# Performance work log

Hardware: AMD Instinct MI355X
Metric: run time of the kernel (lower is better)

The kernel has to match this reference:

```python
import jax, jax.numpy as jnp
import numpy as np

BS, S, D, H, KVH, HD = 2, 2048, 2048, 32, 8, 64
N_REP = H // KVH
N_DOCS = 4


def setup_inputs() -> dict:
    key = jax.random.key(0)
    ks = jax.random.split(key, 7)
    x = jax.random.normal(ks[0], (BS, S, D), dtype=jnp.float32)
    # RoPE table (llama theta=10000), stored as real (cos, sin) pairs: [S, HD//2, 2]
    inv_freq = 1.0 / (10000.0 ** (jnp.arange(0, HD, 2, dtype=jnp.float32) / HD))
    ang = jnp.arange(S, dtype=jnp.float32)[:, None] * inv_freq[None, :]  # [S, HD//2]
    freqs_cis = jnp.stack([jnp.cos(ang), jnp.sin(ang)], axis=-1)
    # packed-document ids, non-decreasing along sequence: [BS, S]
    sequence_id = jnp.sort(
        jax.random.randint(ks[1], (BS, S), 0, N_DOCS, dtype=jnp.int32), axis=-1
    )
    std = 0.02
    wq = jax.random.normal(ks[2], (H * HD, D), dtype=jnp.float32) * std
    wk = jax.random.normal(ks[3], (KVH * HD, D), dtype=jnp.float32) * std
    wv = jax.random.normal(ks[4], (KVH * HD, D), dtype=jnp.float32) * std
    wo = jax.random.normal(ks[5], (D, H * HD), dtype=jnp.float32) * std
    return {"x": x, "freqs_cis": freqs_cis, "sequence_id": sequence_id,
            "wq": wq, "wk": wk, "wv": wv, "wo": wo}


def _apply_rope(t, freqs_cis):
    # t: [b, s, h, hd]; freqs_cis: [s, hd//2, 2] (cos, sin)
    b, s, h, hd = t.shape
    tp = t.reshape(b, s, h, hd // 2, 2)
    t0, t1 = tp[..., 0], tp[..., 1]
    cos = freqs_cis[None, :, None, :, 0]
    sin = freqs_cis[None, :, None, :, 1]
    o0 = t0 * cos - t1 * sin
    o1 = t0 * sin + t1 * cos
    return jnp.stack([o0, o1], axis=-1).reshape(b, s, h, hd)


def reference(x, freqs_cis, sequence_id, wq, wk, wv, wo):
    bs, s, _ = x.shape
    xq = (x @ wq.T).reshape(bs, s, H, HD)
    xk = (x @ wk.T).reshape(bs, s, KVH, HD)
    xv = (x @ wv.T).reshape(bs, s, KVH, HD)
    xq = _apply_rope(xq, freqs_cis)
    xk = _apply_rope(xk, freqs_cis)
    # GQA without materializing repeated KV: group queries by kv head
    q = xq.reshape(bs, s, KVH, N_REP, HD).transpose(0, 2, 3, 1, 4)  # [b,g,r,s,d]
    k = xk.transpose(0, 2, 1, 3)  # [b,g,s,d]
    v = xv.transpose(0, 2, 1, 3)  # [b,g,s,d]
    scale = 1.0 / jnp.sqrt(jnp.float32(HD))
    scores = jnp.einsum("bgrqd,bgkd->bgrqk", q, k) * scale
    # document-causal mask: same sequence_id AND causal
    causal = jnp.tril(jnp.ones((s, s), dtype=bool))
    same_doc = sequence_id[:, :, None] == sequence_id[:, None, :]  # [b,s,s]
    mask = (causal[None] & same_doc)[:, None, None, :, :]  # [b,1,1,s,s]
    scores = jnp.where(mask, scores, jnp.float32(-1e30))
    probs = jax.nn.softmax(scores, axis=-1)
    out = jnp.einsum("bgrqk,bgkd->bgrqd", probs, v)  # [b,g,r,s,d]
    out = out.transpose(0, 3, 1, 2, 4).reshape(bs, s, H * HD)
    return out @ wo.T
```

## Files before the change

### kernel.cpp

```cpp
#include <hip/hip_runtime.h>
#include <hip/hip_bf16.h>

typedef __attribute__((ext_vector_type(8))) short bf16x8;
typedef __attribute__((ext_vector_type(4))) float f32x4;

#define MFMA16(A, B, C) __builtin_amdgcn_mfma_f32_16x16x32_bf16(A, B, C, 0, 0, 0)

__device__ __forceinline__ unsigned short f2bf(float f) {
    unsigned int u = __float_as_uint(f);
    u += 0x7fffu + ((u >> 16) & 1u);
    return (unsigned short)(u >> 16);
}
__device__ __forceinline__ float bf2f(unsigned short h) {
    return __uint_as_float(((unsigned int)h) << 16);
}
__device__ __forceinline__ unsigned int pack_bf2(float lo, float hi) {
    __hip_bfloat162 h = __float22bfloat162_rn(make_float2(lo, hi));
    return *reinterpret_cast<unsigned int*>(&h);
}

__device__ __forceinline__ void gload_lds16(const void* g, void* l) {
    __builtin_amdgcn_global_load_lds(
        (__attribute__((address_space(1))) unsigned int*)g,
        (__attribute__((address_space(3))) unsigned int*)l, 16, 0, 0);
}

__global__ void cvt_kernel(const float* __restrict__ in, unsigned short* __restrict__ out, int n4) {
    const int i = blockIdx.x * 256 + threadIdx.x;
    if (i >= n4) return;
    const float4 v = ((const float4*)in)[i];
    uint2 o;
    o.x = pack_bf2(v.x, v.y);
    o.y = pack_bf2(v.z, v.w);
    ((uint2*)out)[i] = o;
}

__global__ void docstart_kernel(const int* __restrict__ sid, int* __restrict__ ds) {
    const int i = blockIdx.x * 256 + threadIdx.x;
    const int b = i >> 11, s = i & 2047;
    const int* row = sid + b * 2048;
    const int v = row[s];
    int lo = 0, hi = s;
    while (lo < hi) { const int mid = (lo + hi) >> 1; if (row[mid] < v) lo = mid + 1; else hi = mid; }
    ds[i] = lo;
}

template <int EPI>
__global__ __launch_bounds__(256) void gemm_bt(
    const unsigned short* __restrict__ A,
    const unsigned short* __restrict__ B,
    int K, int N,
    unsigned short* __restrict__ oq,
    unsigned short* __restrict__ ok,
    unsigned short* __restrict__ ov,
    float* __restrict__ of)
{
    __shared__ __align__(16) unsigned short sA[128 * 32];
    __shared__ __align__(16) unsigned short sB[128 * 32];
    const int tid = threadIdx.x;
    const int lane = tid & 63, wave = tid >> 6;
    const int wr = wave >> 1, wc = wave & 1;
    const int lr = lane & 15, lc = lane >> 4;

    int bid = blockIdx.y * gridDim.x + blockIdx.x;
    const int cpx = (gridDim.x * gridDim.y) >> 3;
    bid = (bid & 7) * cpx + (bid >> 3);
    const int m0 = (bid / gridDim.x) * 128, n0 = (bid % gridDim.x) * 128;

    f32x4 acc[4][4];
#pragma unroll
    for (int i = 0; i < 4; i++)
#pragma unroll
        for (int j = 0; j < 4; j++) acc[i][j] = (f32x4){0.f, 0.f, 0.f, 0.f};

    const int u0 = tid, u1 = tid + 256;
    for (int k0 = 0; k0 < K; k0 += 32) {
        __syncthreads();
        gload_lds16(A + (size_t)(m0 + (u0 >> 2)) * K + k0 + (u0 & 3) * 8, &sA[u0 * 8]);
        gload_lds16(A + (size_t)(m0 + (u1 >> 2)) * K + k0 + (u1 & 3) * 8, &sA[u1 * 8]);
        gload_lds16(B + (size_t)(n0 + (u0 >> 2)) * K + k0 + (u0 & 3) * 8, &sB[u0 * 8]);
        gload_lds16(B + (size_t)(n0 + (u1 >> 2)) * K + k0 + (u1 & 3) * 8, &sB[u1 * 8]);
        __syncthreads();
        bf16x8 af[4], bfv[4];
#pragma unroll
        for (int i = 0; i < 4; i++) {
            af[i]  = *(const bf16x8*)&sA[(wr * 64 + i * 16 + lr) * 32 + lc * 8];
            bfv[i] = *(const bf16x8*)&sB[(wc * 64 + i * 16 + lr) * 32 + lc * 8];
        }
#pragma unroll
        for (int i = 0; i < 4; i++)
#pragma unroll
            for (int j = 0; j < 4; j++) acc[i][j] = MFMA16(af[i], bfv[j], acc[i][j]);
    }

    if (EPI == 0) {
#pragma unroll
        for (int i = 0; i < 4; i++) {
#pragma unroll
            for (int j = 0; j < 4; j++) {
                const int n = n0 + wc * 64 + j * 16 + lr;
                const int d = n & 63;
#pragma unroll
                for (int r = 0; r < 4; r++) {
                    const int m = m0 + wr * 64 + i * 16 + lc * 4 + r;
                    const int bb = m >> 11, s = m & 2047;
                    const unsigned short val = f2bf(acc[i][j][r]);
                    if (n < 2048) {
                        const int hh = n >> 6;
                        oq[((((size_t)bb * 32 + hh) * 2048 + s) << 6) + d] = val;
                    } else if (n < 2560) {
                        const int hh = (n >> 6) - 32;
                        ok[((((size_t)bb * 8 + hh) * 2048 + s) << 6) + d] = val;
                    } else {
                        const int hh = (n >> 6) - 40;
                        ov[((((size_t)bb * 8 + hh) * 2048 + s) << 6) + d] = val;
                    }
                }
            }
        }
    } else {
#pragma unroll
        for (int i = 0; i < 4; i++)
#pragma unroll
            for (int j = 0; j < 4; j++)
#pragma unroll
                for (int r = 0; r < 4; r++) {
                    const int m = m0 + wr * 64 + i * 16 + lc * 4 + r;
                    const int n = n0 + wc * 64 + j * 16 + lr;
                    of[(size_t)m * N + n] = acc[i][j][r];
                }
    }
}

__global__ void rope_kernel(unsigned short* __restrict__ Qb,
                            unsigned short* __restrict__ Kb,
                            const float* __restrict__ fc)
{
    const int NQ = 2 * 32 * 2048 * 32;
    int i = blockIdx.x * 256 + threadIdx.x;
    unsigned short* base;
    if (i < NQ) base = Qb;
    else { base = Kb; i -= NQ; }
    const int p = i & 31, s = (i >> 5) & 2047, bh = i >> 16;
    const size_t off = (((size_t)bh * 2048 + s) << 6) + p * 2;
    const unsigned int w = *(const unsigned int*)&base[off];
    const float t0 = bf2f((unsigned short)(w & 0xffffu));
    const float t1 = bf2f((unsigned short)(w >> 16));
    const float c = fc[(s * 32 + p) * 2], sn = fc[(s * 32 + p) * 2 + 1];
    *(unsigned int*)&base[off] = pack_bf2(t0 * c - t1 * sn, t0 * sn + t1 * c);
}

__global__ __launch_bounds__(256) void attn_kernel(
    const unsigned short* __restrict__ Q,
    const unsigned short* __restrict__ K,
    const unsigned short* __restrict__ V,
    const int* __restrict__ dstart,
    unsigned short* __restrict__ AO)
{
    const int qt = 31 - blockIdx.x;
    const int h = blockIdx.y, b = blockIdx.z;
    const int kvh = h >> 2;
    const int tid = threadIdx.x, lane = tid & 63, wave = tid >> 6;
    const int lr = lane & 15, lc = lane >> 4;
    const int q0 = qt * 64;
    const int qw = q0 + wave * 16;

    __shared__ __align__(16) unsigned short sK[64 * 64];
    __shared__ __align__(16) unsigned short sVt[64][72];

    const unsigned short* Qh = Q + (((size_t)b * 32 + h) * 2048) * 64;
    const unsigned short* Kh = K + (((size_t)b * 8 + kvh) * 2048) * 64;
    const unsigned short* Vh = V + (((size_t)b * 8 + kvh) * 2048) * 64;

    const bf16x8 qf0 = *(const bf16x8*)&Qh[(size_t)(qw + lr) * 64 + lc * 8];
    const bf16x8 qf1 = *(const bf16x8*)&Qh[(size_t)(qw + lr) * 64 + 32 + lc * 8];

    const int qglob = qw + lr;
    const int dsl = dstart[b * 2048 + qglob];
    const int ds_wmin = dstart[b * 2048 + qw];
    const int t0 = dstart[b * 2048 + q0] & ~63;

    float mrow = -1e30f, lrow = 0.f;
    f32x4 oacc[4];
#pragma unroll
    for (int j = 0; j < 4; j++) oacc[j] = (f32x4){0.f, 0.f, 0.f, 0.f};

    for (int t = t0; t < q0 + 64; t += 64) {
        __syncthreads();
        {
            int slot = tid;
            int r = slot >> 3, c = slot & 7;
            gload_lds16(Kh + (size_t)(t + r) * 64 + ((c ^ (r & 7)) * 8), &sK[slot * 8]);
            slot = tid + 256; r = slot >> 3; c = slot & 7;
            gload_lds16(Kh + (size_t)(t + r) * 64 + ((c ^ (r & 7)) * 8), &sK[slot * 8]);
        }
        {
            const int w8 = wave * 8;
            const uint4 va = *(const uint4*)&Vh[(size_t)(t + lane) * 64 + w8];
            const uint4 vb = *(const uint4*)&Vh[(size_t)(t + lane) * 64 + 32 + w8];
            const unsigned short* pa = (const unsigned short*)&va;
            const unsigned short* pb = (const unsigned short*)&vb;
#pragma unroll
            for (int e = 0; e < 8; e++) sVt[w8 + e][lane] = pa[e];
#pragma unroll
            for (int e = 0; e < 8; e++) sVt[32 + w8 + e][lane] = pb[e];
        }
        asm volatile("s_waitcnt vmcnt(0)" ::: "memory");
        __syncthreads();
        if (t > qw + 15 || t + 63 < ds_wmin) continue;

        f32x4 sc[4];
#pragma unroll
        for (int kk = 0; kk < 4; kk++) {
            const int krow = kk * 16 + lr;
            const bf16x8 kf0 = *(const bf16x8*)&sK[krow * 64 + ((lc ^ (lr & 7)) * 8)];
            const bf16x8 kf1 = *(const bf16x8*)&sK[krow * 64 + (((4 + lc) ^ (lr & 7)) * 8)];
            f32x4 a = (f32x4){0.f, 0.f, 0.f, 0.f};
            a = MFMA16(kf0, qf0, a);
            a = MFMA16(kf1, qf1, a);
            sc[kk] = a;
        }
        float vmax = -3e38f;
#pragma unroll
        for (int kk = 0; kk < 4; kk++)
#pragma unroll
            for (int r = 0; r < 4; r++) {
                const int kpos = t + kk * 16 + lc * 4 + r;
                const bool okm = (kpos <= qglob) && (kpos >= dsl);
                sc[kk][r] = okm ? sc[kk][r] * 0.125f : -3e38f;
                vmax = fmaxf(vmax, sc[kk][r]);
            }
        vmax = fmaxf(vmax, __shfl_xor(vmax, 16));
        vmax = fmaxf(vmax, __shfl_xor(vmax, 32));
        const float mnew = fmaxf(mrow, vmax);
        const float corr = __expf(mrow - mnew);
        mrow = mnew;

        float rsum = 0.f;
        unsigned int pk[4][2];
#pragma unroll
        for (int kk = 0; kk < 4; kk++) {
            const float p0 = __expf(sc[kk][0] - mnew);
            const float p1 = __expf(sc[kk][1] - mnew);
            const float p2 = __expf(sc[kk][2] - mnew);
            const float p3 = __expf(sc[kk][3] - mnew);
            rsum += (p0 + p1) + (p2 + p3);
            pk[kk][0] = pack_bf2(p0, p1);
            pk[kk][1] = pack_bf2(p2, p3);
        }
        rsum += __shfl_xor(rsum, 16);
        rsum += __shfl_xor(rsum, 32);
        lrow = lrow * corr + rsum;
#pragma unroll
        for (int j = 0; j < 4; j++)
#pragma unroll
            for (int r = 0; r < 4; r++) oacc[j][r] *= corr;

        const int srcEven = 32 * (lc & 1) + lr;
        const int srcOdd  = srcEven + 16;
        const bool hiKK = (lc & 2) != 0;
        union { unsigned int w[4]; bf16x8 v; } B0, B1;
        {
            unsigned int a, c;
            a = __shfl(pk[0][0], srcEven); c = __shfl(pk[1][0], srcEven); B0.w[0] = hiKK ? c : a;
            a = __shfl(pk[0][1], srcEven); c = __shfl(pk[1][1], srcEven); B0.w[1] = hiKK ? c : a;
            a = __shfl(pk[0][0], srcOdd);  c = __shfl(pk[1][0], srcOdd);  B0.w[2] = hiKK ? c : a;
            a = __shfl(pk[0][1], srcOdd);  c = __shfl(pk[1][1], srcOdd);  B0.w[3] = hiKK ? c : a;
            a = __shfl(pk[2][0], srcEven); c = __shfl(pk[3][0], srcEven); B1.w[0] = hiKK ? c : a;
            a = __shfl(pk[2][1], srcEven); c = __shfl(pk[3][1], srcEven); B1.w[1] = hiKK ? c : a;
            a = __shfl(pk[2][0], srcOdd);  c = __shfl(pk[3][0], srcOdd);  B1.w[2] = hiKK ? c : a;
            a = __shfl(pk[2][1], srcOdd);  c = __shfl(pk[3][1], srcOdd);  B1.w[3] = hiKK ? c : a;
        }

#pragma unroll
        for (int j = 0; j < 4; j++) {
            const bf16x8 a0 = *(const bf16x8*)&sVt[j * 16 + lr][lc * 8];
            const bf16x8 a1 = *(const bf16x8*)&sVt[j * 16 + lr][32 + lc * 8];
            oacc[j] = MFMA16(a0, B0.v, oacc[j]);
            oacc[j] = MFMA16(a1, B1.v, oacc[j]);
        }
    }

    __syncthreads();
    const float inv = 1.0f / lrow;
#pragma unroll
    for (int j = 0; j < 4; j++)
#pragma unroll
        for (int p = 0; p < 2; p++) {
            const unsigned int w = pack_bf2(oacc[j][2 * p] * inv, oacc[j][2 * p + 1] * inv);
            *(unsigned int*)&sVt[wave * 16 + lr][j * 16 + lc * 4 + 2 * p] = w;
        }
    __syncthreads();
#pragma unroll
    for (int half = 0; half < 2; half++) {
        const int c = lane + 64 * half;
        const int row = c >> 3, ch = c & 7;
        const uint4 o = *(const uint4*)&sVt[wave * 16 + row][ch * 8];
        *(uint4*)&AO[((size_t)b * 2048 + qw + row) * 2048 + h * 64 + ch * 8] = o;
    }
}

extern "C" void kernel_launch(void* const* d_in, const int* in_sizes, int n_in,
                              void* d_out, int out_size, void* d_ws, size_t ws_size,
                              hipStream_t stream) {
    const float* x  = (const float*)d_in[0];
    const float* fc = (const float*)d_in[1];
    const int* sid  = (const int*)d_in[2];
    const float* wq = (const float*)d_in[3];
    const float* wk = (const float*)d_in[4];
    const float* wv = (const float*)d_in[5];
    const float* wo = (const float*)d_in[6];
    float* out = (float*)d_out;

    unsigned short* xb   = (unsigned short*)d_ws;
    unsigned short* wqkv = xb + (size_t)4096 * 2048;
    unsigned short* wob  = wqkv + (size_t)3072 * 2048;
    unsigned short* Qb   = wob + (size_t)2048 * 2048;
    unsigned short* Kb   = Qb + (size_t)2 * 32 * 2048 * 64;
    unsigned short* Vb   = Kb + (size_t)2 * 8 * 2048 * 64;
    unsigned short* AO   = Vb + (size_t)2 * 8 * 2048 * 64;
    int* dstart = (int*)(AO + (size_t)4096 * 2048);

    cvt_kernel<<<8192, 256, 0, stream>>>(x, xb, 2097152);
    cvt_kernel<<<4096, 256, 0, stream>>>(wq, wqkv, 1048576);
    cvt_kernel<<<1024, 256, 0, stream>>>(wk, wqkv + (size_t)2048 * 2048, 262144);
    cvt_kernel<<<1024, 256, 0, stream>>>(wv, wqkv + (size_t)2560 * 2048, 262144);
    cvt_kernel<<<4096, 256, 0, stream>>>(wo, wob, 1048576);
    docstart_kernel<<<16, 256, 0, stream>>>(sid, dstart);
    gemm_bt<0><<<dim3(24, 32), 256, 0, stream>>>(xb, wqkv, 2048, 3072, Qb, Kb, Vb, nullptr);
    rope_kernel<<<20480, 256, 0, stream>>>(Qb, Kb, fc);
    attn_kernel<<<dim3(32, 32, 2), 256, 0, stream>>>(Qb, Kb, Vb, dstart, AO);
    gemm_bt<1><<<dim3(16, 32), 256, 0, stream>>>(AO, wob, 2048, 2048, nullptr, nullptr, nullptr, out);
}
```

Before: 221.1 us.

## Replace QKV projection GEMM with 256x256-tile 8-wave double-buffered kernel

Adds a dedicated QKV projection GEMM that uses 256x256 output tiles, 512 threads and a BK=64 double-buffered LDS pipeline. Global-to-LDS loads use an XOR-swizzled layout, the block index is remapped for locality, and loads are interleaved with four MFMA quadrants per k-step. The goal is more data reuse per tile and overlap of loads with compute, compared with the generic 128x128 gemm_bt. The cost is 128 KB of LDS per block and an intricate hand-placed barrier and vmcnt schedule, with only 192 blocks in the grid.

```diff
diff --git a/kernel.cpp b/kernel.cpp
--- a/kernel.cpp
+++ b/kernel.cpp
@@ -44,6 +44,155 @@
     while (lo < hi) { const int mid = (lo + hi) >> 1; if (row[mid] < v) lo = mid + 1; else hi = mid; }
     ds[i] = lo;
 }
+
+#define QKV_K 2048
+#define QKV_NT 32
+__global__ __launch_bounds__(512, 2) void gemm_qkv8(
+    const unsigned short* __restrict__ A,
+    const unsigned short* __restrict__ B,
+    unsigned short* __restrict__ oq,
+    unsigned short* __restrict__ ok,
+    unsigned short* __restrict__ ov)
+{
+    __shared__ __align__(16) unsigned short S[2][2][2][8192];
+    const int tid = threadIdx.x, lane = tid & 63, w = tid >> 6;
+    const int wr = w >> 2, wc = w & 3;
+    const int lr = lane & 15, lc = lane >> 4;
+
+    int bid = blockIdx.x;
+    bid = (bid & 7) * 24 + (bid >> 3);
+    const int m0 = (bid / 12) * 256, n0 = (bid % 12) * 256;
+
+    const int o0 = (w << 11) + (lane << 4);
+    const int o1 = o0 + 1024;
+    const int v0 = o0 ^ (((o0 >> 9) & 1) << 5);
+    const int v1 = o1 ^ (((o1 >> 9) & 1) << 5);
+    const int r0 = v0 >> 7, c0 = (v0 & 127) >> 1;
+    const int r1 = v1 >> 7, c1 = (v1 & 127) >> 1;
+    const size_t aoff0 = (size_t)(m0 + r0) * QKV_K + c0;
+    const size_t aoff1 = (size_t)(m0 + r1) * QKV_K + c1;
+    const size_t boff0 = (size_t)(n0 + r0) * QKV_K + c0;
+    const size_t boff1 = (size_t)(n0 + r1) * QKV_K + c1;
+    const int d0 = o0 >> 1, d1 = o1 >> 1;
+
+    f32x4 acc[2][2][4][2];
+#pragma unroll
+    for (int a = 0; a < 2; a++)
+#pragma unroll
+        for (int bq = 0; bq < 2; bq++)
+#pragma unroll
+            for (int i = 0; i < 4; i++)
+#pragma unroll
+                for (int j = 0; j < 2; j++) acc[a][bq][i][j] = (f32x4){0.f, 0.f, 0.f, 0.f};
+
+    bf16x8 Af[4][2], Bf0[2][2], Bf1[2][2];
+
+    auto STAGE_A = [&](int bf, int h, int kt) {
+        gload_lds16(A + aoff0 + (size_t)h * 128 * QKV_K + (size_t)kt * 64, &S[bf][0][h][d0]);
+        gload_lds16(A + aoff1 + (size_t)h * 128 * QKV_K + (size_t)kt * 64, &S[bf][0][h][d1]);
+    };
+    auto STAGE_B = [&](int bf, int h, int kt) {
+        gload_lds16(B + boff0 + (size_t)h * 128 * QKV_K + (size_t)kt * 64, &S[bf][1][h][d0]);
+        gload_lds16(B + boff1 + (size_t)h * 128 * QKV_K + (size_t)kt * 64, &S[bf][1][h][d1]);
+    };
+    auto LDA = [&](int bf, int mh) {
+#pragma unroll
+        for (int i = 0; i < 4; i++)
+#pragma unroll
+            for (int kh = 0; kh < 2; kh++) {
+                int by = ((wr * 64 + i * 16 + lr) << 7) + (kh << 6) + (lc << 4);
+                by ^= ((by >> 9) & 1) << 5;
+                Af[i][kh] = *(const bf16x8*)((const char*)&S[bf][0][mh][0] + by);
+            }
+    };
+    auto LDB = [&](int bf, int nh, bf16x8 (&Bf)[2][2]) {
+#pragma unroll
+        for (int j = 0; j < 2; j++)
+#pragma unroll
+            for (int kh = 0; kh < 2; kh++) {
+                int by = ((wc * 32 + j * 16 + lr) << 7) + (kh << 6) + (lc << 4);
+                by ^= ((by >> 9) & 1) << 5;
+                Bf[j][kh] = *(const bf16x8*)((const char*)&S[bf][1][nh][0] + by);
+            }
+    };
+    auto QUAD = [&](f32x4 (&ac)[4][2], bf16x8 (&Bf)[2][2]) {
+        __builtin_amdgcn_s_setprio(1);
+#pragma unroll
+        for (int i = 0; i < 4; i++)
+#pragma unroll
+            for (int j = 0; j < 2; j++)
+#pragma unroll
+                for (int kh = 0; kh < 2; kh++)
+                    ac[i][j] = MFMA16(Af[i][kh], Bf[j][kh], ac[i][j]);
+        __builtin_amdgcn_s_setprio(0);
+    };
+
+#define BAR() __builtin_amdgcn_s_barrier()
+#define LGKM0() asm volatile("s_waitcnt lgkmcnt(0)" ::: "memory")
+
+    STAGE_A(0, 0, 0); STAGE_A(0, 1, 0); STAGE_B(0, 0, 0); STAGE_B(0, 1, 0);
+    STAGE_A(1, 0, 1); STAGE_B(1, 1, 1); STAGE_A(1, 1, 1);
+    asm volatile("s_waitcnt vmcnt(6)" ::: "memory");
+    BAR();
+
+    auto GROUP = [&](int g, int bf) {
+        LDA(bf, 0); LDB(bf, 0, Bf0);
+        if (g + 1 < QKV_NT) STAGE_B(bf ^ 1, 0, g + 1);
+        BAR(); LGKM0();
+        QUAD(acc[0][0], Bf0);
+        BAR();
+        LDB(bf, 1, Bf1);
+        if (g + 2 < QKV_NT) STAGE_A(bf, 0, g + 2);
+        BAR(); LGKM0();
+        QUAD(acc[0][1], Bf1);
+        BAR();
+        LDA(bf, 1);
+        if (g + 2 < QKV_NT) STAGE_B(bf, 1, g + 2);
+        BAR(); LGKM0();
+        QUAD(acc[1][1], Bf1);
+        BAR();
+        if (g + 2 < QKV_NT) STAGE_A(bf, 1, g + 2);
+        BAR();
+        QUAD(acc[1][0], Bf0);
+        if (g == QKV_NT - 2) { asm volatile("s_waitcnt vmcnt(0)" ::: "memory"); }
+        else                 { asm volatile("s_waitcnt vmcnt(6)" ::: "memory"); }
+        BAR();
+    };
+
+#pragma unroll 1
+    for (int g = 0; g < QKV_NT; g += 2) {
+        GROUP(g, 0);
+        GROUP(g + 1, 1);
+    }
+
+#pragma unroll
+    for (int mh = 0; mh < 2; mh++)
+#pragma unroll
+        for (int nh = 0; nh < 2; nh++)
+#pragma unroll
+            for (int i = 0; i < 4; i++)
+#pragma unroll
+                for (int j = 0; j < 2; j++) {
+                    const int n = n0 + nh * 128 + wc * 32 + j * 16 + lr;
+                    const int d = n & 63;
+                    const int hh6 = n >> 6;
+#pragma unroll
+                    for (int r = 0; r < 4; r++) {
+                        const int m = m0 + mh * 128 + wr * 64 + i * 16 + lc * 4 + r;
+                        const int bb = m >> 11, s = m & 2047;
+                        const unsigned short val = f2bf(acc[mh][nh][i][j][r]);
+                        if (n < 2048) {
+                            oq[((((size_t)bb * 32 + hh6) * 2048 + s) << 6) + d] = val;
+                        } else if (n < 2560) {
+                            ok[((((size_t)bb * 8 + (hh6 - 32)) * 2048 + s) << 6) + d] = val;
+                        } else {
+                            ov[((((size_t)bb * 8 + (hh6 - 40)) * 2048 + s) << 6) + d] = val;
+                        }
+                    }
+                }
+}
+#undef BAR
+#undef LGKM0
 
 template <int EPI>
 __global__ __launch_bounds__(256) void gemm_bt(
@@ -327,7 +476,7 @@
     cvt_kernel<<<1024, 256, 0, stream>>>(wv, wqkv + (size_t)2560 * 2048, 262144);
     cvt_kernel<<<4096, 256, 0, stream>>>(wo, wob, 1048576);
     docstart_kernel<<<16, 256, 0, stream>>>(sid, dstart);
-    gemm_bt<0><<<dim3(24, 32), 256, 0, stream>>>(xb, wqkv, 2048, 3072, Qb, Kb, Vb, nullptr);
+    gemm_qkv8<<<dim3(192), 512, 0, stream>>>(xb, wqkv, Qb, Kb, Vb);
     rope_kernel<<<20480, 256, 0, stream>>>(Qb, Kb, fc);
     attn_kernel<<<dim3(32, 32, 2), 256, 0, stream>>>(Qb, Kb, Vb, dstart, AO);
     gemm_bt<1><<<dim3(16, 32), 256, 0, stream>>>(AO, wob, 2048, 2048, nullptr, nullptr, nullptr, out);
```

Measured after the change: 218.3 us. About the same (-1.2%).
